# Kernel optimization log

Hardware: AMD Instinct MI355X
Metric: run time of the kernel (lower is better)

## Reference

```python
import jax, jax.numpy as jnp
import numpy as np

EMB = 1024

def setup_inputs() -> dict:
    key = jax.random.key(0)
    ks = jax.random.split(key, 6)
    B, S, E = 4, 2048, EMB
    x = jax.random.normal(ks[0], (B, S, E), dtype=jnp.float32)
    attention_mask = jax.random.randint(ks[1], (B, S, S), 0, 2, dtype=jnp.int32)
    proj_w = jax.random.normal(ks[2], (E, 3 * E), dtype=jnp.float32) * (1.0 / np.sqrt(E))
    proj_b = jax.random.normal(ks[3], (3 * E,), dtype=jnp.float32) * 0.02
    out_w = jax.random.normal(ks[4], (E, E), dtype=jnp.float32) * (1.0 / np.sqrt(E))
    out_b = jax.random.normal(ks[5], (E,), dtype=jnp.float32) * 0.02
    return {"x": x, "attention_mask": attention_mask, "proj_w": proj_w,
            "proj_b": proj_b, "out_w": out_w, "out_b": out_b}

def reference(x, attention_mask, proj_w, proj_b, out_w, out_b):
    E = x.shape[-1]
    scale = 1.0 / jnp.sqrt(jnp.asarray(E, x.dtype))
    qkv = x @ proj_w + proj_b                      # [B,S,3E]
    q, k, v = jnp.split(qkv, 3, axis=-1)           # each [B,S,E]
    scores = jnp.einsum('bqe,bke->bqk', q, k) * scale  # [B,S,S]
    scores = jnp.where(attention_mask == 0, jnp.asarray(-1e20, scores.dtype), scores)
    attn = jax.nn.softmax(scores, axis=-1)
    ctx = jnp.einsum('bqk,bke->bqe', attn, v)      # [B,S,E]
    return ctx @ out_w + out_b
```

## Files before the change

kernel.cpp:

```cpp
#include <hip/hip_runtime.h>
#include <cstdint>

typedef unsigned short u16;
typedef uint32_t u32;
typedef __bf16 bf16x8 __attribute__((ext_vector_type(8)));
typedef float f32x4 __attribute__((ext_vector_type(4)));

__device__ __forceinline__ u16 f2bf(float f) {
  unsigned u = __float_as_uint(f);
  u += 0x7fffu + ((u >> 16) & 1u);
  return (u16)(u >> 16);
}

__device__ __forceinline__ void async16(const void* g, void* l) {
  __builtin_amdgcn_global_load_lds(
      (const __attribute__((address_space(1))) uint32_t*)g,
      (__attribute__((address_space(3))) uint32_t*)l, 16, 0, 0);
}

__global__ __launch_bounds__(256) void k_prep(const float* __restrict__ x, u16* __restrict__ xb,
                                              const float* __restrict__ pw, u16* __restrict__ wt,
                                              const float* __restrict__ ow, u16* __restrict__ owt,
                                              const int* __restrict__ mask, u32* __restrict__ mbits) {
  const int bid = blockIdx.x;
  if (bid < 8192) {
    const int i = bid * 256 + threadIdx.x;
    const float4 v = ((const float4*)x)[i];
    ushort4 o;
    o.x = f2bf(v.x); o.y = f2bf(v.y); o.z = f2bf(v.z); o.w = f2bf(v.w);
    ((ushort4*)xb)[i] = o;
    return;
  }
  if (bid >= 12288) {
    const size_t w = (size_t)(bid - 12288) * 256 + threadIdx.x;
    const int* p = mask + w * 32;
    u32 bits = 0;
#pragma unroll
    for (int j = 0; j < 8; ++j) {
      const int4 v = ((const int4*)p)[j];
      bits |= (u32)(v.x & 1) << (j * 4 + 0);
      bits |= (u32)(v.y & 1) << (j * 4 + 1);
      bits |= (u32)(v.z & 1) << (j * 4 + 2);
      bits |= (u32)(v.w & 1) << (j * 4 + 3);
    }
    mbits[w] = bits;
    return;
  }
  __shared__ u16 tile[32][33];
  const int tx = threadIdx.x & 31, ty = threadIdx.x >> 5;
  const float* in;
  u16* outp;
  int lda, ldo, c0, r0;
  if (bid < 11264) {
    const int id = bid - 8192;
    c0 = (id % 96) * 32; r0 = (id / 96) * 32;
    in = pw; outp = wt; lda = 3072; ldo = 1024;
  } else {
    const int id = bid - 11264;
    c0 = (id % 32) * 32; r0 = (id / 32) * 32;
    in = ow; outp = owt; lda = 1024; ldo = 1024;
  }
#pragma unroll
  for (int i = 0; i < 4; ++i)
    tile[ty + i * 8][tx] = f2bf(in[(size_t)(r0 + ty + i * 8) * lda + c0 + tx]);
  __syncthreads();
#pragma unroll
  for (int i = 0; i < 4; ++i)
    outp[(size_t)(c0 + ty + i * 8) * ldo + r0 + tx] = tile[tx][ty + i * 8];
}

template <int MODE, int TM, int BN>
__device__ __forceinline__ void gemm_core(
    u16* As, u16* Bs,
    const u16* __restrict__ A, long lda, long bsA,
    const u16* __restrict__ Bt, long ldb, long bsB,
    void* __restrict__ C, long ldc, long bsC,
    int M, int N, int K,
    const float* __restrict__ bias, const u32* __restrict__ mbits,
    int b, int bx, int by) {
  constexpr int MT = TM / 32, NT = BN / 32;
  constexpr int ACALLS = TM / 8, TOT = (TM + BN) / 8, NC = TOT / 4;
  const int m0 = by * TM, n0 = bx * BN;
  const int lane = threadIdx.x & 63;
  const int w = threadIdx.x >> 6;
  const int wr = w >> 1, wc = w & 1;

  const int srow = lane >> 3;
  const int scol = ((lane & 7) ^ ((lane >> 3) & 7)) * 8;
  const u16* pa = A + (size_t)b * bsA + (size_t)(m0 + srow) * lda + scol;
  const u16* pb = Bt + (size_t)b * bsB + (size_t)(n0 + srow) * ldb + scol;

  const int m_l = lane & 15, q = lane >> 4, m7 = m_l & 7;
  const int offs[2] = {(q ^ m7) * 8, ((4 + q) ^ m7) * 8};

  f32x4 acc[MT][NT] = {};
  f32x4 accs[MT] = {};
  bf16x8 ones;
#pragma unroll
  for (int e = 0; e < 8; ++e) ones[e] = (__bf16)1.0f;

  for (int kt = 0; kt < K; kt += 64) {
    __syncthreads();
#pragma unroll
    for (int g = 0; g < NC; ++g) {
      const int idx = w * NC + g;
      if (idx < ACALLS)
        async16(pa + (size_t)(idx * 8) * lda, As + idx * 512);
      else
        async16(pb + (size_t)((idx - ACALLS) * 8) * ldb, Bs + (idx - ACALLS) * 512);
    }
    __syncthreads();
#pragma unroll
    for (int s = 0; s < 2; ++s) {
      bf16x8 af[MT], bfr[NT];
#pragma unroll
      for (int t = 0; t < MT; ++t)
        af[t] = *(const bf16x8*)(As + (wr * (TM / 2) + t * 16 + m_l) * 64 + offs[s]);
#pragma unroll
      for (int t = 0; t < NT; ++t)
        bfr[t] = *(const bf16x8*)(Bs + (wc * (BN / 2) + t * 16 + m_l) * 64 + offs[s]);
#pragma unroll
      for (int mt = 0; mt < MT; ++mt)
#pragma unroll
        for (int nt = 0; nt < NT; ++nt)
          acc[mt][nt] = __builtin_amdgcn_mfma_f32_16x16x32_bf16(af[mt], bfr[nt], acc[mt][nt], 0, 0, 0);
      if constexpr (MODE == 2) {
#pragma unroll
        for (int mt = 0; mt < MT; ++mt)
          accs[mt] = __builtin_amdgcn_mfma_f32_16x16x32_bf16(af[mt], ones, accs[mt], 0, 0, 0);
      }
    }
    pa += 64;
    pb += 64;
  }

  if constexpr (MODE == 1) {
    __syncthreads();
    const int rl = threadIdx.x >> 1, pr = threadIdx.x & 1;
    const uint2 v = *(const uint2*)(mbits + ((size_t)(b * M + m0 + rl)) * (N >> 5) + (n0 >> 5) + pr * 2);
    ((u32*)As)[rl * 4 + pr * 2] = v.x;
    ((u32*)As)[rl * 4 + pr * 2 + 1] = v.y;
    __syncthreads();
  }

  float rinv[MT][4];
  if constexpr (MODE == 2) {
#pragma unroll
    for (int mt = 0; mt < MT; ++mt)
#pragma unroll
      for (int r = 0; r < 4; ++r) rinv[mt][r] = 1.0f / accs[mt][r];
  }

#pragma unroll
  for (int mt = 0; mt < MT; ++mt) {
#pragma unroll
    for (int nt = 0; nt < NT; ++nt) {
      const int col = n0 + wc * (BN / 2) + nt * 16 + m_l;
      const int row0 = m0 + wr * (TM / 2) + mt * 16 + q * 4;
      if constexpr (MODE == 3) {
        ushort4 o;
        o.x = f2bf(acc[mt][nt][0]); o.y = f2bf(acc[mt][nt][1]);
        o.z = f2bf(acc[mt][nt][2]); o.w = f2bf(acc[mt][nt][3]);
        *(ushort4*)((u16*)C + (size_t)b * bsC + (size_t)col * ldc + row0) = o;
      } else {
#pragma unroll
        for (int r = 0; r < 4; ++r) {
          const int row = row0 + r;
          float v = acc[mt][nt][r];
          if constexpr (MODE == 0) {
            v += bias[col];
            if (col < 1024) v *= 0.03125f;
            ((u16*)C)[(size_t)b * bsC + (size_t)row * ldc + col] = f2bf(v);
          } else if constexpr (MODE == 1) {
            const int cl = wc * 64 + nt * 16 + m_l;
            const int rl = wr * 64 + mt * 16 + q * 4 + r;
            const u32 wb = ((const u32*)As)[rl * 4 + (cl >> 5)];
            v = ((wb >> (cl & 31)) & 1u) ? __expf(fminf(v, 30.f)) : 0.f;
            ((u16*)C)[(size_t)b * bsC + (size_t)row * ldc + col] = f2bf(v);
          } else if constexpr (MODE == 2) {
            v = v * rinv[mt][r] + bias[col];
            ((float*)C)[(size_t)b * bsC + (size_t)row * ldc + col] = v;
          }
        }
      }
    }
  }
}

template <int MODE, int TM, int BN, bool SWZ>
__global__ __launch_bounds__(256) void gemm_bt(
    const u16* __restrict__ A, long lda, long bsA,
    const u16* __restrict__ Bt, long ldb, long bsB,
    void* __restrict__ C, long ldc, long bsC,
    int M, int N, int K,
    const float* __restrict__ bias, const u32* __restrict__ mbits) {
  __shared__ u16 As[TM * 64];
  __shared__ u16 Bs[BN * 64];
  int bx = blockIdx.x, by = blockIdx.y, bz = blockIdx.z;
  if constexpr (SWZ) {
    const int gx = gridDim.x, gxy = gridDim.x * gridDim.y;
    const int T = gxy * gridDim.z;
    int L = bx + gx * by + gxy * bz;
    L = (L & 7) * (T >> 3) + (L >> 3);
    bz = L / gxy;
    const int r = L % gxy;
    bx = r % gx;
    by = r / gx;
  }
  gemm_core<MODE, TM, BN>(As, Bs, A, lda, bsA, Bt, ldb, bsB, C, ldc, bsC, M, N, K,
                          bias, mbits, bz, bx, by);
}

extern "C" void kernel_launch(void* const* d_in, const int* in_sizes, int n_in,
                              void* d_out, int out_size, void* d_ws, size_t ws_size,
                              hipStream_t stream) {
  const float* x = (const float*)d_in[0];
  const int* mask = (const int*)d_in[1];
  const float* proj_w = (const float*)d_in[2];
  const float* proj_b = (const float*)d_in[3];
  const float* out_w = (const float*)d_in[4];
  const float* out_b = (const float*)d_in[5];
  float* out = (float*)d_out;

  char* ws = (char*)d_ws;
  u16* xb = (u16*)(ws);
  u16* wt = (u16*)(ws + 16777216);
  u16* owt = (u16*)(ws + 23068672);
  u16* qkv = (u16*)(ws + 25165824);
  u16* P = (u16*)(ws + 75497472);
  u32* mbits = (u32*)(ws + 109051904);
  u16* Ut = (u16*)xb;

  k_prep<<<14336, 256, 0, stream>>>(x, xb, proj_w, wt, out_w, owt, mask, mbits);
  gemm_bt<0, 128, 128, false><<<dim3(24, 64, 1), 256, 0, stream>>>(
      xb, 1024, 0, wt, 1024, 0, qkv, 3072, 0, 8192, 3072, 1024, proj_b, nullptr);
  gemm_bt<1, 128, 128, true><<<dim3(16, 16, 4), 256, 0, stream>>>(
      qkv, 3072, (long)2048 * 3072, qkv + 1024, 3072, (long)2048 * 3072,
      P, 2048, (long)2048 * 2048, 2048, 2048, 1024, nullptr, mbits);
  gemm_bt<3, 64, 128, true><<<dim3(8, 32, 4), 256, 0, stream>>>(
      qkv + 2048, 3072, (long)2048 * 3072, owt, 1024, 0,
      Ut, 2048, (long)1024 * 2048, 2048, 1024, 1024, nullptr, nullptr);
  gemm_bt<2, 128, 128, true><<<dim3(8, 16, 4), 256, 0, stream>>>(
      P, 2048, (long)2048 * 2048, Ut, 2048, (long)1024 * 2048,
      out, 1024, (long)2048 * 1024, 2048, 1024, 2048, out_b, nullptr);
}
```

Measured before the change: 341.9 us.

## Compute softmax row sums in exp epilogue via atomics instead of ones-MFMA

Removes the extra MFMA against a ones vector that the final GEMM used to build softmax denominators. The exp-producing score GEMM now reduces each row's partial sum across lanes and atomically adds it into a zeroed workspace buffer. The final GEMM reads those sums from memory. The QKV projection GEMM also switches to swizzled block ordering. This adds atomics and a zeroing pass, and the normalization now uses fp32 exp sums rather than sums of the bf16-rounded P.

```diff
diff --git a/kernel.cpp b/kernel.cpp
--- a/kernel.cpp
+++ b/kernel.cpp
@@ -21,8 +21,14 @@
 __global__ __launch_bounds__(256) void k_prep(const float* __restrict__ x, u16* __restrict__ xb,
                                               const float* __restrict__ pw, u16* __restrict__ wt,
                                               const float* __restrict__ ow, u16* __restrict__ owt,
-                                              const int* __restrict__ mask, u32* __restrict__ mbits) {
+                                              const int* __restrict__ mask, u32* __restrict__ mbits,
+                                              float* __restrict__ lsum) {
   const int bid = blockIdx.x;
+  if (bid >= 14336) {
+    const int i = (bid - 14336) * 256 + threadIdx.x;
+    ((float4*)lsum)[i] = make_float4(0.f, 0.f, 0.f, 0.f);
+    return;
+  }
   if (bid < 8192) {
     const int i = bid * 256 + threadIdx.x;
     const float4 v = ((const float4*)x)[i];
@@ -77,6 +83,7 @@
     void* __restrict__ C, long ldc, long bsC,
     int M, int N, int K,
     const float* __restrict__ bias, const u32* __restrict__ mbits,
+    float* __restrict__ lsum,
     int b, int bx, int by) {
   constexpr int MT = TM / 32, NT = BN / 32;
   constexpr int ACALLS = TM / 8, TOT = (TM + BN) / 8, NC = TOT / 4;
@@ -94,10 +101,6 @@
   const int offs[2] = {(q ^ m7) * 8, ((4 + q) ^ m7) * 8};
 
   f32x4 acc[MT][NT] = {};
-  f32x4 accs[MT] = {};
-  bf16x8 ones;
-#pragma unroll
-  for (int e = 0; e < 8; ++e) ones[e] = (__bf16)1.0f;
 
   for (int kt = 0; kt < K; kt += 64) {
     __syncthreads();
@@ -124,11 +127,6 @@
 #pragma unroll
         for (int nt = 0; nt < NT; ++nt)
           acc[mt][nt] = __builtin_amdgcn_mfma_f32_16x16x32_bf16(af[mt], bfr[nt], acc[mt][nt], 0, 0, 0);
-      if constexpr (MODE == 2) {
-#pragma unroll
-        for (int mt = 0; mt < MT; ++mt)
-          accs[mt] = __builtin_amdgcn_mfma_f32_16x16x32_bf16(af[mt], ones, accs[mt], 0, 0, 0);
-      }
     }
     pa += 64;
     pb += 64;
@@ -145,10 +143,24 @@
 
   float rinv[MT][4];
   if constexpr (MODE == 2) {
+    __syncthreads();
+    if (threadIdx.x < TM)
+      ((float*)Bs)[threadIdx.x] = lsum[(size_t)b * M + m0 + threadIdx.x];
+    __syncthreads();
+#pragma unroll
+    for (int mt = 0; mt < MT; ++mt) {
+      const f32x4 sv = *(const f32x4*)((const float*)Bs + wr * (TM / 2) + mt * 16 + q * 4);
+#pragma unroll
+      for (int r = 0; r < 4; ++r) rinv[mt][r] = 1.0f / sv[r];
+    }
+  }
+
+  float rsum[MT][4];
+  if constexpr (MODE == 1) {
 #pragma unroll
     for (int mt = 0; mt < MT; ++mt)
 #pragma unroll
-      for (int r = 0; r < 4; ++r) rinv[mt][r] = 1.0f / accs[mt][r];
+      for (int r = 0; r < 4; ++r) rsum[mt][r] = 0.f;
   }
 
 #pragma unroll
@@ -172,10 +184,11 @@
             if (col < 1024) v *= 0.03125f;
             ((u16*)C)[(size_t)b * bsC + (size_t)row * ldc + col] = f2bf(v);
           } else if constexpr (MODE == 1) {
-            const int cl = wc * 64 + nt * 16 + m_l;
-            const int rl = wr * 64 + mt * 16 + q * 4 + r;
+            const int cl = wc * (BN / 2) + nt * 16 + m_l;
+            const int rl = wr * (TM / 2) + mt * 16 + q * 4 + r;
             const u32 wb = ((const u32*)As)[rl * 4 + (cl >> 5)];
             v = ((wb >> (cl & 31)) & 1u) ? __expf(fminf(v, 30.f)) : 0.f;
+            rsum[mt][r] += v;
             ((u16*)C)[(size_t)b * bsC + (size_t)row * ldc + col] = f2bf(v);
           } else if constexpr (MODE == 2) {
             v = v * rinv[mt][r] + bias[col];
@@ -185,6 +198,21 @@
       }
     }
   }
+
+  if constexpr (MODE == 1) {
+#pragma unroll
+    for (int mt = 0; mt < MT; ++mt)
+#pragma unroll
+      for (int r = 0; r < 4; ++r) {
+        float s = rsum[mt][r];
+        s += __shfl_xor(s, 1, 64);
+        s += __shfl_xor(s, 2, 64);
+        s += __shfl_xor(s, 4, 64);
+        s += __shfl_xor(s, 8, 64);
+        if (m_l == 0)
+          atomicAdd(&lsum[(size_t)b * M + m0 + wr * (TM / 2) + mt * 16 + q * 4 + r], s);
+      }
+  }
 }
 
 template <int MODE, int TM, int BN, bool SWZ>
@@ -193,7 +221,8 @@
     const u16* __restrict__ Bt, long ldb, long bsB,
     void* __restrict__ C, long ldc, long bsC,
     int M, int N, int K,
-    const float* __restrict__ bias, const u32* __restrict__ mbits) {
+    const float* __restrict__ bias, const u32* __restrict__ mbits,
+    float* __restrict__ lsum) {
   __shared__ u16 As[TM * 64];
   __shared__ u16 Bs[BN * 64];
   int bx = blockIdx.x, by = blockIdx.y, bz = blockIdx.z;
@@ -208,7 +237,7 @@
     by = r / gx;
   }
   gemm_core<MODE, TM, BN>(As, Bs, A, lda, bsA, Bt, ldb, bsB, C, ldc, bsC, M, N, K,
-                          bias, mbits, bz, bx, by);
+                          bias, mbits, lsum, bz, bx, by);
 }
 
 extern "C" void kernel_launch(void* const* d_in, const int* in_sizes, int n_in,
@@ -229,18 +258,19 @@
   u16* qkv = (u16*)(ws + 25165824);
   u16* P = (u16*)(ws + 75497472);
   u32* mbits = (u32*)(ws + 109051904);
+  float* lsum = (float*)(ws + 111149056);
   u16* Ut = (u16*)xb;
 
-  k_prep<<<14336, 256, 0, stream>>>(x, xb, proj_w, wt, out_w, owt, mask, mbits);
-  gemm_bt<0, 128, 128, false><<<dim3(24, 64, 1), 256, 0, stream>>>(
-      xb, 1024, 0, wt, 1024, 0, qkv, 3072, 0, 8192, 3072, 1024, proj_b, nullptr);
+  k_prep<<<14344, 256, 0, stream>>>(x, xb, proj_w, wt, out_w, owt, mask, mbits, lsum);
+  gemm_bt<0, 128, 128, true><<<dim3(24, 64, 1), 256, 0, stream>>>(
+      xb, 1024, 0, wt, 1024, 0, qkv, 3072, 0, 8192, 3072, 1024, proj_b, nullptr, nullptr);
   gemm_bt<1, 128, 128, true><<<dim3(16, 16, 4), 256, 0, stream>>>(
       qkv, 3072, (long)2048 * 3072, qkv + 1024, 3072, (long)2048 * 3072,
-      P, 2048, (long)2048 * 2048, 2048, 2048, 1024, nullptr, mbits);
+      P, 2048, (long)2048 * 2048, 2048, 2048, 1024, nullptr, mbits, lsum);
   gemm_bt<3, 64, 128, true><<<dim3(8, 32, 4), 256, 0, stream>>>(
       qkv + 2048, 3072, (long)2048 * 3072, owt, 1024, 0,
-      Ut, 2048, (long)1024 * 2048, 2048, 1024, 1024, nullptr, nullptr);
+      Ut, 2048, (long)1024 * 2048, 2048, 1024, 1024, nullptr, nullptr, nullptr);
   gemm_bt<2, 128, 128, true><<<dim3(8, 16, 4), 256, 0, stream>>>(
       P, 2048, (long)2048 * 2048, Ut, 2048, (long)1024 * 2048,
-      out, 1024, (long)2048 * 1024, 2048, 1024, 2048, out_b, nullptr);
-}
+      out, 1024, (long)2048 * 1024, 2048, 1024, 2048, out_b, nullptr, lsum);
+}
```

New measurement: 339.7 us. No clear change (-0.7%).
